# Kernel tuning notes

Hardware: AMD Instinct MI355X
Metric: run time of the kernel (lower is better)

The kernel has to match this reference:

```python
import jax, jax.numpy as jnp
import numpy as np


def grid_sample_bilinear(feat, grid):
    """Bilinear grid_sample, align_corners=False, zeros padding.
    feat: [B, C, H, W]; grid: [B, N, 2] with (x, y) in [-1, 1]. Returns [B, C, N].
    """
    B, C, H, W = feat.shape
    gx, gy = grid[..., 0], grid[..., 1]
    # unnormalize (align_corners=False): pixel = ((g + 1) * size - 1) / 2
    ix = ((gx + 1.0) * W - 1.0) * 0.5
    iy = ((gy + 1.0) * H - 1.0) * 0.5
    x0 = jnp.floor(ix)
    y0 = jnp.floor(iy)
    x1 = x0 + 1.0
    y1 = y0 + 1.0
    wx1 = ix - x0
    wx0 = 1.0 - wx1
    wy1 = iy - y0
    wy0 = 1.0 - wy1
    featf = feat.reshape(B, C, H * W)

    def corner(xi, yi, w):
        valid = (xi >= 0) & (xi <= W - 1) & (yi >= 0) & (yi <= H - 1)
        xi_c = jnp.clip(xi, 0, W - 1).astype(jnp.int32)
        yi_c = jnp.clip(yi, 0, H - 1).astype(jnp.int32)
        idx = yi_c * W + xi_c                                  # [B, N]
        vals = jnp.take_along_axis(featf, idx[:, None, :], axis=2)  # [B, C, N]
        return vals * (w * valid.astype(feat.dtype))[:, None, :]

    return (corner(x0, y0, wx0 * wy0) + corner(x1, y0, wx1 * wy0)
            + corner(x0, y1, wx0 * wy1) + corner(x1, y1, wx1 * wy1))


def setup_inputs() -> dict:
    key = jax.random.key(0)
    ks = jax.random.split(key, 8)
    B_T, C, H, W = 128, 256, 64, 64
    J = 17
    n_heads, n_points = 8, 4
    HP = n_heads * n_points
    video_features = jax.random.normal(ks[0], (B_T, C, H, W), dtype=jnp.float32)
    reference_points = jax.random.uniform(ks[1], (B_T, J, 2), dtype=jnp.float32,
                                          minval=-1.0, maxval=1.0)
    # offset predictor: Linear(C -> HP*2); weights init small like the module
    W_off = 0.01 * jax.random.normal(ks[2], (C, HP * 2), dtype=jnp.float32)
    b_off = 0.01 * jax.random.normal(ks[3], (HP * 2,), dtype=jnp.float32)
    # weight predictor: Linear(C -> HP)
    W_w = 0.01 * jax.random.normal(ks[4], (C, HP), dtype=jnp.float32)
    b_w = jnp.zeros((HP,), dtype=jnp.float32)
    # output projection: Linear(C -> C), xavier-ish scale
    W_out = jax.random.normal(ks[5], (C, C), dtype=jnp.float32) * (1.0 / np.sqrt(C))
    b_out = jnp.zeros((C,), dtype=jnp.float32)
    return {"video_features": video_features, "reference_points": reference_points,
            "W_off": W_off, "b_off": b_off, "W_w": W_w, "b_w": b_w,
            "W_out": W_out, "b_out": b_out}


def reference(video_features, reference_points, W_off, b_off, W_w, b_w, W_out, b_out):
    B, C, H, W = video_features.shape
    J = reference_points.shape[1]
    HP = W_w.shape[1]  # n_heads * n_points
    # initial queries: sample features at reference points -> [B, J, C]
    q = grid_sample_bilinear(video_features, reference_points).transpose(0, 2, 1)
    # learned fractional offsets: [B, J, HP, 2]
    offsets = (q @ W_off + b_off).reshape(B, J, HP, 2)
    # softmax attention weights over all heads*points: [B, J, HP]
    weights = jax.nn.softmax(q @ W_w + b_w, axis=-1)
    # final sampling grid, clamped to valid range: [B, J*HP, 2]
    grid = jnp.clip(reference_points[:, :, None, :] + offsets, -1.0, 1.0)
    grid = grid.reshape(B, J * HP, 2)
    # sample and weighted-sum: [B, C, J, HP] x [B, J, HP] -> [B, J, C]
    sampled = grid_sample_bilinear(video_features, grid).reshape(B, C, J, HP)
    out = jnp.einsum('bcjp,bjp->bjc', sampled, weights)
    return out @ W_out + b_out
```

## Files before the change

kernel.cpp:

```cpp
#include <hip/hip_runtime.h>

#define B_  128
#define C_  256
#define H_  64
#define W_  64
#define J_  17
#define HP_ 32
#define HW_ (H_ * W_)
#define CG_ 2

__global__ __launch_bounds__(256)
void pass12_kernel(const float* __restrict__ feat,
                   const float* __restrict__ refpts,
                   const float* __restrict__ Woff,
                   const float* __restrict__ boff,
                   const float* __restrict__ Ww,
                   const float* __restrict__ bw,
                   int4*  __restrict__ meta_idx,
                   float4* __restrict__ meta_w)
{
    __shared__ float q_lds[C_];
    __shared__ float part_off[4][64];
    __shared__ float part_w[4][32];
    __shared__ float off_lds[2 * HP_];
    __shared__ float logit_lds[HP_];

    const int bj = blockIdx.x;
    const int b  = bj / J_;
    const int j  = bj % J_;
    const int c  = threadIdx.x;

    const float rx = refpts[(b * J_ + j) * 2 + 0];
    const float ry = refpts[(b * J_ + j) * 2 + 1];

    {
        const float* featbc = feat + (size_t)(b * C_ + c) * HW_;
        float ix = (rx + 1.0f) * (0.5f * W_) - 0.5f;
        float iy = (ry + 1.0f) * (0.5f * H_) - 0.5f;
        float x0f = floorf(ix), y0f = floorf(iy);
        int x0 = (int)x0f, y0 = (int)y0f;
        int x1 = x0 + 1,  y1 = y0 + 1;
        float wx1 = ix - x0f, wx0 = 1.0f - wx1;
        float wy1 = iy - y0f, wy0 = 1.0f - wy1;
        bool vx0 = (x0 >= 0) && (x0 < W_);
        bool vx1 = (x1 >= 0) && (x1 < W_);
        bool vy0 = (y0 >= 0) && (y0 < H_);
        bool vy1 = (y1 >= 0) && (y1 < H_);
        int x0c = min(max(x0, 0), W_ - 1), x1c = min(max(x1, 0), W_ - 1);
        int y0c = min(max(y0, 0), H_ - 1), y1c = min(max(y1, 0), H_ - 1);
        float v00 = (vx0 && vy0) ? featbc[y0c * W_ + x0c] : 0.0f;
        float v10 = (vx1 && vy0) ? featbc[y0c * W_ + x1c] : 0.0f;
        float v01 = (vx0 && vy1) ? featbc[y1c * W_ + x0c] : 0.0f;
        float v11 = (vx1 && vy1) ? featbc[y1c * W_ + x1c] : 0.0f;
        q_lds[c] = v00 * (wx0 * wy0) + v10 * (wx1 * wy0)
                 + v01 * (wx0 * wy1) + v11 * (wx1 * wy1);
    }
    __syncthreads();

    {
        const int wv = c >> 6, ln = c & 63;
        float aoff = 0.0f, aw = 0.0f;
        #pragma unroll 8
        for (int i = 0; i < 64; ++i) {
            const int k = wv * 64 + i;
            const float qv = q_lds[k];
            aoff += qv * Woff[k * 64 + ln];
            if (ln < 32) aw += qv * Ww[k * 32 + ln];
        }
        part_off[wv][ln] = aoff;
        if (ln < 32) part_w[wv][ln] = aw;
    }
    __syncthreads();
    if (c < 64) {
        off_lds[c] = boff[c] + part_off[0][c] + part_off[1][c]
                   + part_off[2][c] + part_off[3][c];
    } else if (c < 96) {
        const int p = c - 64;
        logit_lds[p] = bw[p] + part_w[0][p] + part_w[1][p]
                     + part_w[2][p] + part_w[3][p];
    }
    __syncthreads();

    if (c < HP_) {
        float l = logit_lds[c];
        float m = l;
        #pragma unroll
        for (int mask = 16; mask >= 1; mask >>= 1) m = fmaxf(m, __shfl_xor(m, mask));
        float e = expf(l - m);
        float s = e;
        #pragma unroll
        for (int mask = 16; mask >= 1; mask >>= 1) s += __shfl_xor(s, mask);
        const float ww = e / s;

        float gx = fminf(fmaxf(rx + off_lds[2 * c + 0], -1.0f), 1.0f);
        float gy = fminf(fmaxf(ry + off_lds[2 * c + 1], -1.0f), 1.0f);
        float ix = (gx + 1.0f) * (0.5f * W_) - 0.5f;
        float iy = (gy + 1.0f) * (0.5f * H_) - 0.5f;
        float x0f = floorf(ix), y0f = floorf(iy);
        int x0 = (int)x0f, y0 = (int)y0f;
        int x1 = x0 + 1,  y1 = y0 + 1;
        float wx1 = ix - x0f, wx0 = 1.0f - wx1;
        float wy1 = iy - y0f, wy0 = 1.0f - wy1;
        float v00 = (float)((x0 >= 0) && (x0 < W_) && (y0 >= 0) && (y0 < H_));
        float v10 = (float)((x1 >= 0) && (x1 < W_) && (y0 >= 0) && (y0 < H_));
        float v01 = (float)((x0 >= 0) && (x0 < W_) && (y1 >= 0) && (y1 < H_));
        float v11 = (float)((x1 >= 0) && (x1 < W_) && (y1 >= 0) && (y1 < H_));
        int x0c = min(max(x0, 0), W_ - 1), x1c = min(max(x1, 0), W_ - 1);
        int y0c = min(max(y0, 0), H_ - 1), y1c = min(max(y1, 0), H_ - 1);
        const int mi = bj * HP_ + c;
        meta_idx[mi] = make_int4(y0c * W_ + x0c, y0c * W_ + x1c,
                                 y1c * W_ + x0c, y1c * W_ + x1c);
        meta_w[mi] = make_float4(ww * wx0 * wy0 * v00, ww * wx1 * wy0 * v10,
                                 ww * wx0 * wy1 * v01, ww * wx1 * wy1 * v11);
    }
}

__global__ __launch_bounds__(256)
void gather_kernel(const float* __restrict__ feat,
                   const int4*  __restrict__ meta_idx,
                   const float4* __restrict__ meta_w,
                   float* __restrict__ acc)
{
    __shared__ float plane[CG_ * HW_];

    const int blk = blockIdx.x;
    const int b   = blk >> 7;
    const int cg  = blk & 127;
    const int c0  = cg * CG_;
    const int t   = threadIdx.x;

    {
        const float4* src = (const float4*)(feat + (size_t)(b * C_ + c0) * HW_);
        float4* dst = (float4*)plane;
        #pragma unroll
        for (int i = 0; i < 8; ++i)
            dst[t + i * 256] = src[t + i * 256];
    }
    __syncthreads();

    const int wv   = t >> 6;
    const int ln   = t & 63;
    const int p    = ln & 31;
    const int half = ln >> 5;

    #pragma unroll
    for (int iter = 0; iter < 3; ++iter) {
        const int j = iter * 8 + wv * 2 + half;
        float pj0 = 0.0f, pj1 = 0.0f;
        if (j < J_) {
            const int mi = (b * J_ + j) * HP_ + p;
            const int4   id = meta_idx[mi];
            const float4 w  = meta_w[mi];
            pj0 = w.x * plane[id.x] + w.y * plane[id.y]
                + w.z * plane[id.z] + w.w * plane[id.w];
            pj1 = w.x * plane[HW_ + id.x] + w.y * plane[HW_ + id.y]
                + w.z * plane[HW_ + id.z] + w.w * plane[HW_ + id.w];
        }
        #pragma unroll
        for (int mask = 16; mask >= 1; mask >>= 1) {
            pj0 += __shfl_xor(pj0, mask);
            pj1 += __shfl_xor(pj1, mask);
        }
        if (j < J_ && p == 0) {
            float2* dst = (float2*)(acc + ((size_t)(b * J_ + j)) * C_ + c0);
            *dst = make_float2(pj0, pj1);
        }
    }
}

__global__ __launch_bounds__(256)
void proj_kernel(const float* __restrict__ acc,
                 const float* __restrict__ Wout,
                 const float* __restrict__ bout,
                 float* __restrict__ out)
{
    __shared__ float a_lds[C_];
    __shared__ float partial[4][C_];
    const int bj = blockIdx.x;
    const int t  = threadIdx.x;
    a_lds[t] = acc[(size_t)bj * C_ + t];
    __syncthreads();

    const int wv = t >> 6, ln = t & 63;
    float s0 = 0.0f, s1 = 0.0f, s2 = 0.0f, s3 = 0.0f;
    #pragma unroll 8
    for (int i = 0; i < 64; ++i) {
        const int k = wv * 64 + i;
        const float qv = a_lds[k];
        const float* row = Wout + (size_t)k * C_;
        s0 += qv * row[ln];
        s1 += qv * row[ln + 64];
        s2 += qv * row[ln + 128];
        s3 += qv * row[ln + 192];
    }
    partial[wv][ln]       = s0;
    partial[wv][ln + 64]  = s1;
    partial[wv][ln + 128] = s2;
    partial[wv][ln + 192] = s3;
    __syncthreads();

    float o = bout[t] + partial[0][t] + partial[1][t] + partial[2][t] + partial[3][t];
    out[(size_t)bj * C_ + t] = o;
}

__device__ __forceinline__ float bilin_sample(const float* __restrict__ featc,
                                              float gx, float gy) {
    float ix = (gx + 1.0f) * (0.5f * W_) - 0.5f;
    float iy = (gy + 1.0f) * (0.5f * H_) - 0.5f;
    float x0f = floorf(ix), y0f = floorf(iy);
    int x0 = (int)x0f, y0 = (int)y0f;
    int x1 = x0 + 1,  y1 = y0 + 1;
    float wx1 = ix - x0f, wx0 = 1.0f - wx1;
    float wy1 = iy - y0f, wy0 = 1.0f - wy1;
    bool vx0 = (x0 >= 0) && (x0 < W_);
    bool vx1 = (x1 >= 0) && (x1 < W_);
    bool vy0 = (y0 >= 0) && (y0 < H_);
    bool vy1 = (y1 >= 0) && (y1 < H_);
    int x0c = min(max(x0, 0), W_ - 1), x1c = min(max(x1, 0), W_ - 1);
    int y0c = min(max(y0, 0), H_ - 1), y1c = min(max(y1, 0), H_ - 1);
    float v00 = (vx0 && vy0) ? featc[y0c * W_ + x0c] : 0.0f;
    float v10 = (vx1 && vy0) ? featc[y0c * W_ + x1c] : 0.0f;
    float v01 = (vx0 && vy1) ? featc[y1c * W_ + x0c] : 0.0f;
    float v11 = (vx1 && vy1) ? featc[y1c * W_ + x1c] : 0.0f;
    return v00 * (wx0 * wy0) + v10 * (wx1 * wy0)
         + v01 * (wx0 * wy1) + v11 * (wx1 * wy1);
}

__global__ __launch_bounds__(256)
void msdks_kernel(const float* __restrict__ feat,
                  const float* __restrict__ refpts,
                  const float* __restrict__ Woff,
                  const float* __restrict__ boff,
                  const float* __restrict__ Ww,
                  const float* __restrict__ bw,
                  const float* __restrict__ Wout,
                  const float* __restrict__ bout,
                  float* __restrict__ out)
{
    __shared__ float q_lds[C_];
    __shared__ float off_lds[2 * HP_];
    __shared__ float logit_lds[HP_];
    __shared__ float wgt_lds[HP_];
    __shared__ float gx_lds[HP_];
    __shared__ float gy_lds[HP_];
    __shared__ float acc_lds[C_];

    const int bj = blockIdx.x;
    const int b  = bj / J_;
    const int j  = bj % J_;
    const int c  = threadIdx.x;

    const float rx = refpts[(b * J_ + j) * 2 + 0];
    const float ry = refpts[(b * J_ + j) * 2 + 1];
    const float* featbc = feat + (size_t)(b * C_ + c) * HW_;

    q_lds[c] = bilin_sample(featbc, rx, ry);
    __syncthreads();

    if (c < 64) {
        float s = boff[c];
        for (int k = 0; k < C_; ++k) s += q_lds[k] * Woff[k * 64 + c];
        off_lds[c] = s;
    } else if (c < 96) {
        const int p = c - 64;
        float s = bw[p];
        for (int k = 0; k < C_; ++k) s += q_lds[k] * Ww[k * HP_ + p];
        logit_lds[p] = s;
    }
    __syncthreads();

    if (c < HP_) {
        float l = logit_lds[c];
        float m = l;
        for (int mask = 16; mask; mask >>= 1) m = fmaxf(m, __shfl_xor(m, mask));
        float e = expf(l - m);
        float s = e;
        for (int mask = 16; mask; mask >>= 1) s += __shfl_xor(s, mask);
        wgt_lds[c] = e / s;
        gx_lds[c] = fminf(fmaxf(rx + off_lds[c * 2 + 0], -1.0f), 1.0f);
        gy_lds[c] = fminf(fmaxf(ry + off_lds[c * 2 + 1], -1.0f), 1.0f);
    }
    __syncthreads();

    float acc = 0.0f;
    for (int pp = 0; pp < HP_; ++pp)
        acc += wgt_lds[pp] * bilin_sample(featbc, gx_lds[pp], gy_lds[pp]);
    acc_lds[c] = acc;
    __syncthreads();

    float o = bout[c];
    for (int k = 0; k < C_; ++k) o += acc_lds[k] * Wout[k * C_ + c];
    out[(size_t)(b * J_ + j) * C_ + c] = o;
}

extern "C" void kernel_launch(void* const* d_in, const int* in_sizes, int n_in,
                              void* d_out, int out_size, void* d_ws, size_t ws_size,
                              hipStream_t stream) {
    const float* feat   = (const float*)d_in[0];
    const float* refpts = (const float*)d_in[1];
    const float* Woff   = (const float*)d_in[2];
    const float* boff   = (const float*)d_in[3];
    const float* Ww     = (const float*)d_in[4];
    const float* bw     = (const float*)d_in[5];
    const float* Wout   = (const float*)d_in[6];
    const float* bout   = (const float*)d_in[7];
    float* out = (float*)d_out;

    const size_t n_meta    = (size_t)B_ * J_ * HP_;
    const size_t idx_bytes = n_meta * sizeof(int4);
    const size_t w_bytes   = n_meta * sizeof(float4);
    const size_t acc_bytes = (size_t)B_ * J_ * C_ * sizeof(float);

    if (ws_size >= idx_bytes + w_bytes + acc_bytes) {
        char* ws = (char*)d_ws;
        int4*   meta_idx = (int4*)ws;
        float4* meta_w   = (float4*)(ws + idx_bytes);
        float*  acc      = (float*)(ws + idx_bytes + w_bytes);

        pass12_kernel<<<dim3(B_ * J_), dim3(256), 0, stream>>>(
            feat, refpts, Woff, boff, Ww, bw, meta_idx, meta_w);
        gather_kernel<<<dim3(B_ * (C_ / CG_)), dim3(256), 0, stream>>>(
            feat, meta_idx, meta_w, acc);
        proj_kernel<<<dim3(B_ * J_), dim3(256), 0, stream>>>(
            acc, Wout, bout, out);
    } else {
        msdks_kernel<<<dim3(B_ * J_), dim3(256), 0, stream>>>(
            feat, refpts, Woff, boff, Ww, bw, Wout, bout, out);
    }
}
```

Before: 177.5 us.

## Use direct global-to-LDS loads in gather, batch rows in projection, split weight GEMV

The gather kernel now loads each feature plane through global_load_lds, which writes global memory straight into LDS without passing through registers. It also prefetches the per-sample metadata before the barrier so those loads overlap the plane copy. The projection kernel processes 8 output rows per block, so each Wout element is read once and reused across all 8 rows, with no cross-wave reduction. In the pass12 kernel the attention-weight GEMV is spread over all lanes instead of half of them. The risks are more registers per thread in proj, fewer proj blocks, and reliance on the alignment that global_load_lds requires.

```diff
diff --git a/kernel.cpp b/kernel.cpp
--- a/kernel.cpp
+++ b/kernel.cpp
@@ -21,7 +21,7 @@
 {
     __shared__ float q_lds[C_];
     __shared__ float part_off[4][64];
-    __shared__ float part_w[4][32];
+    __shared__ float part_w[8][32];
     __shared__ float off_lds[2 * HP_];
     __shared__ float logit_lds[HP_];
 
@@ -59,16 +59,21 @@
 
     {
         const int wv = c >> 6, ln = c & 63;
-        float aoff = 0.0f, aw = 0.0f;
+        float aoff = 0.0f;
         #pragma unroll 8
         for (int i = 0; i < 64; ++i) {
             const int k = wv * 64 + i;
-            const float qv = q_lds[k];
-            aoff += qv * Woff[k * 64 + ln];
-            if (ln < 32) aw += qv * Ww[k * 32 + ln];
+            aoff += q_lds[k] * Woff[k * 64 + ln];
         }
         part_off[wv][ln] = aoff;
-        if (ln < 32) part_w[wv][ln] = aw;
+        const int h = ln >> 5, p = ln & 31;
+        float aw = 0.0f;
+        #pragma unroll 8
+        for (int i = 0; i < 32; ++i) {
+            const int k = wv * 64 + h * 32 + i;
+            aw += q_lds[k] * Ww[k * 32 + p];
+        }
+        part_w[wv * 2 + h][p] = aw;
     }
     __syncthreads();
     if (c < 64) {
@@ -76,8 +81,10 @@
                    + part_off[2][c] + part_off[3][c];
     } else if (c < 96) {
         const int p = c - 64;
-        logit_lds[p] = bw[p] + part_w[0][p] + part_w[1][p]
-                     + part_w[2][p] + part_w[3][p];
+        float s = bw[p];
+        #pragma unroll
+        for (int sidx = 0; sidx < 8; ++sidx) s += part_w[sidx][p];
+        logit_lds[p] = s;
     }
     __syncthreads();
 
@@ -128,34 +135,48 @@
     const int cg  = blk & 127;
     const int c0  = cg * CG_;
     const int t   = threadIdx.x;
+    const int wv  = t >> 6;
+    const int ln  = t & 63;
 
     {
-        const float4* src = (const float4*)(feat + (size_t)(b * C_ + c0) * HW_);
-        float4* dst = (float4*)plane;
-        #pragma unroll
-        for (int i = 0; i < 8; ++i)
-            dst[t + i * 256] = src[t + i * 256];
-    }
-    __syncthreads();
-
-    const int wv   = t >> 6;
-    const int ln   = t & 63;
+        const char* gsrc = (const char*)(feat + (size_t)(b * C_ + c0) * HW_);
+        #pragma unroll
+        for (int i = 0; i < 8; ++i) {
+            const size_t off = ((size_t)(i * 256 + wv * 64)) * 16;
+            __builtin_amdgcn_global_load_lds(
+                (const __attribute__((address_space(1))) void*)(gsrc + off + (size_t)ln * 16),
+                (__attribute__((address_space(3))) void*)((char*)plane + off),
+                16, 0, 0);
+        }
+    }
+
     const int p    = ln & 31;
     const int half = ln >> 5;
-
+    int4   id_r[3];
+    float4 w_r[3];
     #pragma unroll
     for (int iter = 0; iter < 3; ++iter) {
         const int j = iter * 8 + wv * 2 + half;
-        float pj0 = 0.0f, pj1 = 0.0f;
         if (j < J_) {
             const int mi = (b * J_ + j) * HP_ + p;
-            const int4   id = meta_idx[mi];
-            const float4 w  = meta_w[mi];
-            pj0 = w.x * plane[id.x] + w.y * plane[id.y]
-                + w.z * plane[id.z] + w.w * plane[id.w];
-            pj1 = w.x * plane[HW_ + id.x] + w.y * plane[HW_ + id.y]
-                + w.z * plane[HW_ + id.z] + w.w * plane[HW_ + id.w];
-        }
+            id_r[iter] = meta_idx[mi];
+            w_r[iter]  = meta_w[mi];
+        } else {
+            id_r[iter] = make_int4(0, 0, 0, 0);
+            w_r[iter]  = make_float4(0.f, 0.f, 0.f, 0.f);
+        }
+    }
+    __syncthreads();
+
+    #pragma unroll
+    for (int iter = 0; iter < 3; ++iter) {
+        const int j = iter * 8 + wv * 2 + half;
+        const int4   id = id_r[iter];
+        const float4 w  = w_r[iter];
+        float pj0 = w.x * plane[id.x] + w.y * plane[id.y]
+                  + w.z * plane[id.z] + w.w * plane[id.w];
+        float pj1 = w.x * plane[HW_ + id.x] + w.y * plane[HW_ + id.y]
+                  + w.z * plane[HW_ + id.z] + w.w * plane[HW_ + id.w];
         #pragma unroll
         for (int mask = 16; mask >= 1; mask >>= 1) {
             pj0 += __shfl_xor(pj0, mask);
@@ -168,39 +189,39 @@
     }
 }
 
+#define PROJ_ROWS 8
 __global__ __launch_bounds__(256)
 void proj_kernel(const float* __restrict__ acc,
                  const float* __restrict__ Wout,
                  const float* __restrict__ bout,
                  float* __restrict__ out)
 {
-    __shared__ float a_lds[C_];
-    __shared__ float partial[4][C_];
-    const int bj = blockIdx.x;
-    const int t  = threadIdx.x;
-    a_lds[t] = acc[(size_t)bj * C_ + t];
-    __syncthreads();
-
-    const int wv = t >> 6, ln = t & 63;
-    float s0 = 0.0f, s1 = 0.0f, s2 = 0.0f, s3 = 0.0f;
-    #pragma unroll 8
-    for (int i = 0; i < 64; ++i) {
-        const int k = wv * 64 + i;
-        const float qv = a_lds[k];
-        const float* row = Wout + (size_t)k * C_;
-        s0 += qv * row[ln];
-        s1 += qv * row[ln + 64];
-        s2 += qv * row[ln + 128];
-        s3 += qv * row[ln + 192];
-    }
-    partial[wv][ln]       = s0;
-    partial[wv][ln + 64]  = s1;
-    partial[wv][ln + 128] = s2;
-    partial[wv][ln + 192] = s3;
-    __syncthreads();
-
-    float o = bout[t] + partial[0][t] + partial[1][t] + partial[2][t] + partial[3][t];
-    out[(size_t)bj * C_ + t] = o;
+    __shared__ float a_lds[PROJ_ROWS][C_];
+    const int bj0 = blockIdx.x * PROJ_ROWS;
+    const int t   = threadIdx.x;
+
+    #pragma unroll
+    for (int r = 0; r < PROJ_ROWS; ++r)
+        a_lds[r][t] = acc[(size_t)(bj0 + r) * C_ + t];
+    __syncthreads();
+
+    const int c = t;
+    float o[PROJ_ROWS];
+    const float bb = bout[c];
+    #pragma unroll
+    for (int r = 0; r < PROJ_ROWS; ++r) o[r] = bb;
+
+    #pragma unroll 4
+    for (int k = 0; k < C_; ++k) {
+        const float wv = Wout[(size_t)k * C_ + c];
+        #pragma unroll
+        for (int r = 0; r < PROJ_ROWS; ++r)
+            o[r] += a_lds[r][k] * wv;
+    }
+
+    #pragma unroll
+    for (int r = 0; r < PROJ_ROWS; ++r)
+        out[(size_t)(bj0 + r) * C_ + c] = o[r];
 }
 
 __device__ __forceinline__ float bilin_sample(const float* __restrict__ featc,
@@ -321,7 +342,7 @@
             feat, refpts, Woff, boff, Ww, bw, meta_idx, meta_w);
         gather_kernel<<<dim3(B_ * (C_ / CG_)), dim3(256), 0, stream>>>(
             feat, meta_idx, meta_w, acc);
-        proj_kernel<<<dim3(B_ * J_), dim3(256), 0, stream>>>(
+        proj_kernel<<<dim3((B_ * J_) / PROJ_ROWS), dim3(256), 0, stream>>>(
             acc, Wout, bout, out);
     } else {
         msdks_kernel<<<dim3(B_ * J_), dim3(256), 0, stream>>>(
```

After: 162.2 us. 1.09x faster.
